# Optimization experiments

Measured on AMD Instinct MI355X. Metric: run time of the kernel, lower is better.

The kernel has to match this reference:

```python
import jax, jax.numpy as jnp
import numpy as np

N_EMBD = 768
N_HEAD = 12
HEAD_DIM = N_EMBD // N_HEAD


def setup_inputs() -> dict:
    key = jax.random.key(0)
    ks = jax.random.split(key, 5)
    B, T, C = 1, 4096, N_EMBD
    s = 1.0 / np.sqrt(C)
    return {
        "x": jax.random.normal(ks[0], (B, T, C), dtype=jnp.float32),
        "wq": jax.random.normal(ks[1], (C, C), dtype=jnp.float32) * s,
        "wk": jax.random.normal(ks[2], (C, C), dtype=jnp.float32) * s,
        "wv": jax.random.normal(ks[3], (C, C), dtype=jnp.float32) * s,
        "wo": jax.random.normal(ks[4], (C, C), dtype=jnp.float32) * s,
    }


def reference(x, wq, wk, wv, wo):
    B, T, C = x.shape
    H, D = N_HEAD, HEAD_DIM
    # projections: torch Linear(y = x @ W^T); weights stored as (out, in)
    q = (x @ wq.T).reshape(B, T, H, D).transpose(0, 2, 1, 3)  # B H T D
    k = (x @ wk.T).reshape(B, T, H, D).transpose(0, 2, 1, 3)
    v = (x @ wv.T).reshape(B, T, H, D).transpose(0, 2, 1, 3)
    scale = 1.0 / jnp.sqrt(jnp.asarray(D, dtype=x.dtype))
    attn = jnp.einsum("bhtd,bhsd->bhts", q, k) * scale  # B H T T
    causal = jnp.tril(jnp.ones((T, T), dtype=bool))
    attn = jnp.where(causal, attn, -jnp.inf)
    attn = jax.nn.softmax(attn, axis=-1)
    out = jnp.einsum("bhts,bhsd->bhtd", attn, v)  # B H T D
    out = out.transpose(0, 2, 1, 3).reshape(B, T, C)
    return out @ wo.T
```

## Files before the change

kernel.cpp:

```cpp
#include <hip/hip_runtime.h>


#define T_SEQ 4096
#define C_EMB 768
#define NH    12
#define HD    64

typedef __attribute__((ext_vector_type(8))) short bf16x8;
typedef __attribute__((ext_vector_type(4))) float floatx4;

#define QSCALE 0.18033688011112042f

__device__ __forceinline__ unsigned short f2bf(float f) {
  union { float f; unsigned u; } v; v.f = f;
  unsigned r = v.u + 0x7fffu + ((v.u >> 16) & 1u);
  return (unsigned short)(r >> 16);
}
__device__ __forceinline__ unsigned short f2bf_rhu(float f) {
  union { float f; unsigned u; } v; v.f = f;
  return (unsigned short)((v.u + 0x8000u) >> 16);
}
__device__ __forceinline__ float bf2f(unsigned short h) {
  union { unsigned u; float f; } v; v.u = ((unsigned)h) << 16;
  return v.f;
}

__device__ __forceinline__ void gload_lds16(const void* gptr, void* ldsptr) {
  __builtin_amdgcn_global_load_lds(
      (const __attribute__((address_space(1))) unsigned int*)gptr,
      (__attribute__((address_space(3))) unsigned int*)ldsptr,
      16, 0, 0);
}

__global__ void cast_all_kernel(const float* __restrict__ x,
                                const float* __restrict__ wq,
                                const float* __restrict__ wk,
                                const float* __restrict__ wv,
                                const float* __restrict__ wo,
                                unsigned short* __restrict__ dst) {
  const int GX = (T_SEQ * C_EMB) / 4;
  const int GW = (C_EMB * C_EMB) / 4;
  int i = blockIdx.x * blockDim.x + threadIdx.x;
  const float* src; int local;
  if (i < GX) { src = x; local = i; }
  else {
    int t = i - GX; int w = t / GW; local = t - w * GW;
    src = (w == 0) ? wq : (w == 1) ? wk : (w == 2) ? wv : wo;
  }
  float4 f = reinterpret_cast<const float4*>(src)[local];
  ushort4 u;
  u.x = f2bf(f.x); u.y = f2bf(f.y); u.z = f2bf(f.z); u.w = f2bf(f.w);
  reinterpret_cast<ushort4*>(dst)[i] = u;
}

__global__ __launch_bounds__(256) void gemm_qkv(
    const unsigned short* __restrict__ A,
    const unsigned short* __restrict__ B,
    unsigned short* __restrict__ Qb,
    unsigned short* __restrict__ Kb,
    unsigned short* __restrict__ Vt) {
  constexpr int K = 768, BM = 128, BK = 32;
  __shared__ __align__(16) unsigned short As[BM * BK];
  __shared__ __align__(16) unsigned short Bs[BM * BK];
  const int tid = threadIdx.x;
  const int wave = tid >> 6, lane = tid & 63;
  const int lm = lane & 15, lq = lane >> 4;
  const int sw2 = (lm ^ (lm >> 2)) & 3;
  const int m0 = blockIdx.x * BM, n0 = blockIdx.y * BM;
  const int wm = (wave & 1) * 64, wn = (wave >> 1) * 64;
  floatx4 acc[4][4] = {};

  for (int k0 = 0; k0 < K; k0 += BK) {
#pragma unroll
    for (int i = 0; i < 2; i++) {
      int idx = (wave * 2 + i) * 64 + lane;
      int row = idx >> 2;
      int ch = (idx & 3) ^ ((row ^ (row >> 2)) & 3);
      gload_lds16(A + (size_t)(m0 + row) * K + k0 + ch * 8, (char*)As + idx * 16);
      gload_lds16(B + (size_t)(n0 + row) * K + k0 + ch * 8, (char*)Bs + idx * 16);
    }
    __syncthreads();
    bf16x8 af[4], bfr[4];
#pragma unroll
    for (int i = 0; i < 4; i++)
      af[i] = *(const bf16x8*)(As + (wm + i * 16 + lm) * BK + ((lq ^ sw2) * 8));
#pragma unroll
    for (int j = 0; j < 4; j++)
      bfr[j] = *(const bf16x8*)(Bs + (wn + j * 16 + lm) * BK + ((lq ^ sw2) * 8));
#pragma unroll
    for (int i = 0; i < 4; i++)
#pragma unroll
      for (int j = 0; j < 4; j++)
        acc[i][j] = __builtin_amdgcn_mfma_f32_16x16x32_bf16(af[i], bfr[j], acc[i][j], 0, 0, 0);
    __syncthreads();
  }

  const int which = n0 / C_EMB;
  if (which < 2) {
    unsigned short* tgt = (which == 0) ? Qb : Kb;
    const float sc = (which == 0) ? QSCALE : 1.0f;
#pragma unroll
    for (int i = 0; i < 4; i++)
#pragma unroll
      for (int j = 0; j < 4; j++) {
        int n = n0 - which * C_EMB + wn + j * 16 + lm;
        int h = n >> 6, d = n & 63;
#pragma unroll
        for (int r = 0; r < 4; r++) {
          int m = m0 + wm + i * 16 + lq * 4 + r;
          tgt[(((size_t)h * T_SEQ + m) << 6) + d] = f2bf(acc[i][j][r] * sc);
        }
      }
  } else {
#pragma unroll
    for (int i = 0; i < 4; i++)
#pragma unroll
      for (int j = 0; j < 4; j++) {
        int n = n0 - 2 * C_EMB + wn + j * 16 + lm;
        int h = n >> 6, d = n & 63;
        int m = m0 + wm + i * 16 + lq * 4;
        ushort4 pk;
        pk.x = f2bf(acc[i][j][0]); pk.y = f2bf(acc[i][j][1]);
        pk.z = f2bf(acc[i][j][2]); pk.w = f2bf(acc[i][j][3]);
        *(ushort4*)(Vt + ((size_t)(h * HD + d)) * T_SEQ + m) = pk;
      }
  }
}

__global__ __launch_bounds__(256, 4) void attn_kernel(
    const unsigned short* __restrict__ Q,
    const unsigned short* __restrict__ K,
    const unsigned short* __restrict__ Vt,
    unsigned short* __restrict__ Op0,
    unsigned short* __restrict__ Op1,
    float* __restrict__ lpart) {
  constexpr int BS = 64, PS = 72;
  __shared__ __align__(16) unsigned short Ks[BS * HD];
  __shared__ __align__(16) unsigned short Vs[HD * BS];
  __shared__ __align__(16) unsigned short Ps[4 * 32 * PS];
  const int bid = blockIdx.x;
  const int h = bid % NH;
  const int z = bid / NH;
  const int qt = (T_SEQ / 128 - 1) - (z >> 1);
  const int c = z & 1;
  const int q0 = qt * 128;
  const int sb = c ? (qt + 1) : 0;
  const int se = c ? (2 * qt + 2) : (qt + 1);

  const int tid = threadIdx.x;
  const int wave = tid >> 6, lane = tid & 63;
  const int lm = lane & 15, lq = lane >> 4;
  const unsigned short* Qh = Q + (size_t)h * T_SEQ * HD;
  const unsigned short* Kh = K + (size_t)h * T_SEQ * HD;
  const unsigned short* Vh = Vt + (size_t)h * HD * T_SEQ;
  const int qrow_base = q0 + wave * 32;
  unsigned short* Pw = Ps + wave * 32 * PS;
  const int swz = lm & 7;

  bf16x8 qf[2][2];
#pragma unroll
  for (int m = 0; m < 2; m++)
#pragma unroll
    for (int kk = 0; kk < 2; kk++)
      qf[m][kk] = *(const bf16x8*)(Qh + (size_t)(qrow_base + m * 16 + lm) * HD + kk * 32 + lq * 8);

  float rsum[2][4] = {};
  floatx4 o_acc[2][4] = {};

  auto stage = [&](int s0) {
#pragma unroll
    for (int i = 0; i < 2; i++) {
      int idx = (wave * 2 + i) * 64 + lane;
      int row = idx >> 3;
      int ch = (idx & 7) ^ (row & 7);
      gload_lds16(Kh + (size_t)(s0 + row) * HD + ch * 8, (char*)Ks + idx * 16);
      gload_lds16(Vh + (size_t)row * T_SEQ + s0 + ch * 8, (char*)Vs + idx * 16);
    }
  };

  stage(sb * BS);
  for (int it = sb; it < se; ++it) {
    const int s0 = it * BS;
    __syncthreads();

    floatx4 sa[2][4] = {};
#pragma unroll
    for (int kk = 0; kk < 2; kk++)
#pragma unroll
      for (int j = 0; j < 4; j++) {
        int row = j * 16 + lm;
        bf16x8 kf = *(const bf16x8*)(Ks + (row * 8 + ((kk * 4 + lq) ^ swz)) * 8);
#pragma unroll
        for (int m = 0; m < 2; m++)
          sa[m][j] = __builtin_amdgcn_mfma_f32_16x16x32_bf16(qf[m][kk], kf, sa[m][j], 0, 0, 0);
      }

    if (s0 >= q0) {
#pragma unroll
      for (int m = 0; m < 2; m++)
#pragma unroll
        for (int j = 0; j < 4; j++) {
          int scol = s0 + j * 16 + lm;
#pragma unroll
          for (int r = 0; r < 4; r++) {
            int qrow = qrow_base + m * 16 + lq * 4 + r;
            if (scol > qrow) sa[m][j][r] = -1e30f;
          }
        }
    }

#pragma unroll
    for (int m = 0; m < 2; m++)
#pragma unroll
      for (int j = 0; j < 4; j++)
#pragma unroll
        for (int r = 0; r < 4; r++) {
          float p = __builtin_amdgcn_exp2f(sa[m][j][r]);
          rsum[m][r] += p;
          Pw[(m * 16 + lq * 4 + r) * PS + j * 16 + lm] = f2bf_rhu(p);
        }

#pragma unroll
    for (int kk = 0; kk < 2; kk++) {
      bf16x8 pf[2];
#pragma unroll
      for (int m = 0; m < 2; m++)
        pf[m] = *(const bf16x8*)(Pw + (m * 16 + lm) * PS + kk * 32 + lq * 8);
#pragma unroll
      for (int jd = 0; jd < 4; jd++) {
        int row = jd * 16 + lm;
        bf16x8 vf = *(const bf16x8*)(Vs + (row * 8 + ((kk * 4 + lq) ^ swz)) * 8);
#pragma unroll
        for (int m = 0; m < 2; m++)
          o_acc[m][jd] = __builtin_amdgcn_mfma_f32_16x16x32_bf16(pf[m], vf, o_acc[m][jd], 0, 0, 0);
      }
    }

    if (it + 1 < se) {
      __syncthreads();
      stage(s0 + BS);
    }
  }

  unsigned short* Oc = c ? Op1 : Op0;
  float* lc = lpart + (size_t)c * NH * T_SEQ;
#pragma unroll
  for (int m = 0; m < 2; m++)
#pragma unroll
    for (int r = 0; r < 4; r++) {
      float s = rsum[m][r];
      s += __shfl_xor(s, 1);
      s += __shfl_xor(s, 2);
      s += __shfl_xor(s, 4);
      s += __shfl_xor(s, 8);
      int t = qrow_base + m * 16 + lq * 4 + r;
      if (lm == 0) lc[h * T_SEQ + t] = s;
#pragma unroll
      for (int jd = 0; jd < 4; jd++)
        Oc[((size_t)h * T_SEQ + t) * HD + jd * 16 + lm] = f2bf(o_acc[m][jd][r]);
    }
}

__global__ void combine_kernel(const unsigned short* __restrict__ Op0,
                               const unsigned short* __restrict__ Op1,
                               const float* __restrict__ lpart,
                               unsigned short* __restrict__ Ob) {
  int idx = blockIdx.x * blockDim.x + threadIdx.x;
  int d4 = idx & 15;
  int t = (idx >> 4) & (T_SEQ - 1);
  int h = idx >> 16;
  float l = lpart[h * T_SEQ + t] + lpart[NH * T_SEQ + h * T_SEQ + t];
  float inv = 1.0f / l;
  ushort4 a = reinterpret_cast<const ushort4*>(Op0)[idx];
  ushort4 b = reinterpret_cast<const ushort4*>(Op1)[idx];
  ushort4 u;
  u.x = f2bf((bf2f(a.x) + bf2f(b.x)) * inv);
  u.y = f2bf((bf2f(a.y) + bf2f(b.y)) * inv);
  u.z = f2bf((bf2f(a.z) + bf2f(b.z)) * inv);
  u.w = f2bf((bf2f(a.w) + bf2f(b.w)) * inv);
  *(ushort4*)(Ob + (size_t)t * C_EMB + h * HD + d4 * 4) = u;
}

__global__ __launch_bounds__(256) void gemm_out(
    const unsigned short* __restrict__ A,
    const unsigned short* __restrict__ B,
    float* __restrict__ Out) {
  constexpr int K = 768, BM = 128, BK = 32;
  __shared__ __align__(16) unsigned short As[BM * BK];
  __shared__ __align__(16) unsigned short Bs[BM * BK];
  const int tid = threadIdx.x;
  const int wave = tid >> 6, lane = tid & 63;
  const int lm = lane & 15, lq = lane >> 4;
  const int sw2 = (lm ^ (lm >> 2)) & 3;
  const int m0 = blockIdx.x * BM, n0 = blockIdx.y * BM;
  const int wm = (wave & 1) * 64, wn = (wave >> 1) * 64;
  floatx4 acc[4][4] = {};

  for (int k0 = 0; k0 < K; k0 += BK) {
#pragma unroll
    for (int i = 0; i < 2; i++) {
      int idx = (wave * 2 + i) * 64 + lane;
      int row = idx >> 2;
      int ch = (idx & 3) ^ ((row ^ (row >> 2)) & 3);
      gload_lds16(A + (size_t)(m0 + row) * K + k0 + ch * 8, (char*)As + idx * 16);
      gload_lds16(B + (size_t)(n0 + row) * K + k0 + ch * 8, (char*)Bs + idx * 16);
    }
    __syncthreads();
    bf16x8 af[4], bfr[4];
#pragma unroll
    for (int i = 0; i < 4; i++)
      af[i] = *(const bf16x8*)(As + (wm + i * 16 + lm) * BK + ((lq ^ sw2) * 8));
#pragma unroll
    for (int j = 0; j < 4; j++)
      bfr[j] = *(const bf16x8*)(Bs + (wn + j * 16 + lm) * BK + ((lq ^ sw2) * 8));
#pragma unroll
    for (int i = 0; i < 4; i++)
#pragma unroll
      for (int j = 0; j < 4; j++)
        acc[i][j] = __builtin_amdgcn_mfma_f32_16x16x32_bf16(af[i], bfr[j], acc[i][j], 0, 0, 0);
    __syncthreads();
  }
#pragma unroll
  for (int i = 0; i < 4; i++)
#pragma unroll
    for (int j = 0; j < 4; j++)
#pragma unroll
      for (int r = 0; r < 4; r++) {
        int m = m0 + wm + i * 16 + lq * 4 + r;
        int n = n0 + wn + j * 16 + lm;
        Out[(size_t)m * C_EMB + n] = acc[i][j][r];
      }
}

extern "C" void kernel_launch(void* const* d_in, const int* in_sizes, int n_in,
                              void* d_out, int out_size, void* d_ws, size_t ws_size,
                              hipStream_t stream) {
  const float* x  = (const float*)d_in[0];
  const float* wq = (const float*)d_in[1];
  const float* wk = (const float*)d_in[2];
  const float* wv = (const float*)d_in[3];
  const float* wo = (const float*)d_in[4];
  float* out = (float*)d_out;

  const size_t XN = (size_t)T_SEQ * C_EMB;
  const size_t WN = (size_t)C_EMB * C_EMB;
  unsigned short* base = (unsigned short*)d_ws;

  unsigned short* Xb   = base;
  unsigned short* Wqkv = base + XN;
  unsigned short* Wob  = base + XN + 3 * WN;
  unsigned short* Qb   = base + XN + 4 * WN;
  unsigned short* Kb   = Qb + XN;
  unsigned short* Vt   = Kb + XN;
  unsigned short* Op1  = Vt + XN;
  unsigned short* Op0  = base;
  float* lpart = (float*)(base + XN);
  unsigned short* Ob   = Qb;

  const int ngroups = (int)((XN + 4 * WN) / 4);
  cast_all_kernel<<<dim3(ngroups / 256), 256, 0, stream>>>(x, wq, wk, wv, wo, Xb);

  gemm_qkv<<<dim3(T_SEQ / 128, 2304 / 128), 256, 0, stream>>>(Xb, Wqkv, Qb, Kb, Vt);

  attn_kernel<<<dim3((T_SEQ / 128) * 2 * NH), 256, 0, stream>>>(Qb, Kb, Vt, Op0, Op1, lpart);
  combine_kernel<<<dim3((int)(XN / 4) / 256), 256, 0, stream>>>(Op0, Op1, lpart, Ob);
  gemm_out<<<dim3(T_SEQ / 128, C_EMB / 128), 256, 0, stream>>>(Ob, Wob, out);
}
```

Baseline: 189.2 us.

## Split causal attention KV range into four chunks with fp32 partials

The attention kernel now splits each query tile's key range into four chunks instead of two, launching twice as many blocks. Each chunk writes fp32 partial outputs and row sums, and a new combine kernel adds the non-empty chunks and normalises. The aim is better load balance and occupancy across CUs for the causal workload. In exchange the partials move more memory traffic (fp32, four copies) and need a larger workspace, with a fallback to the old two-way path when the workspace is too small.

```diff
diff --git a/kernel.cpp b/kernel.cpp
--- a/kernel.cpp
+++ b/kernel.cpp
@@ -127,7 +127,133 @@
   }
 }
 
-__global__ __launch_bounds__(256, 4) void attn_kernel(
+struct AttnState {
+  float rsum[2][4];
+  floatx4 o_acc[2][4];
+};
+
+template <typename EpilogueFn>
+__device__ __forceinline__ void attn_body(
+    const unsigned short* __restrict__ Q,
+    const unsigned short* __restrict__ K,
+    const unsigned short* __restrict__ Vt,
+    int h, int q0, int sb, int se,
+    unsigned short* Ks, unsigned short* Vs, unsigned short* Ps,
+    EpilogueFn epi) {
+  constexpr int BS = 64, PS = 72;
+  const int tid = threadIdx.x;
+  const int wave = tid >> 6, lane = tid & 63;
+  const int lm = lane & 15, lq = lane >> 4;
+  const unsigned short* Qh = Q + (size_t)h * T_SEQ * HD;
+  const unsigned short* Kh = K + (size_t)h * T_SEQ * HD;
+  const unsigned short* Vh = Vt + (size_t)h * HD * T_SEQ;
+  const int qrow_base = q0 + wave * 32;
+  unsigned short* Pw = Ps + wave * 32 * PS;
+  const int swz = lm & 7;
+
+  bf16x8 qf[2][2];
+#pragma unroll
+  for (int m = 0; m < 2; m++)
+#pragma unroll
+    for (int kk = 0; kk < 2; kk++)
+      qf[m][kk] = *(const bf16x8*)(Qh + (size_t)(qrow_base + m * 16 + lm) * HD + kk * 32 + lq * 8);
+
+  AttnState st;
+#pragma unroll
+  for (int m = 0; m < 2; m++)
+#pragma unroll
+    for (int r = 0; r < 4; r++) { st.rsum[m][r] = 0.f; st.o_acc[m][r] = floatx4{0.f,0.f,0.f,0.f}; }
+
+  auto stage = [&](int s0) {
+#pragma unroll
+    for (int i = 0; i < 2; i++) {
+      int idx = (wave * 2 + i) * 64 + lane;
+      int row = idx >> 3;
+      int ch = (idx & 7) ^ (row & 7);
+      gload_lds16(Kh + (size_t)(s0 + row) * HD + ch * 8, (char*)Ks + idx * 16);
+      gload_lds16(Vh + (size_t)row * T_SEQ + s0 + ch * 8, (char*)Vs + idx * 16);
+    }
+  };
+
+  stage(sb * BS);
+  for (int it = sb; it < se; ++it) {
+    const int s0 = it * BS;
+    __syncthreads();
+
+    floatx4 sa[2][4] = {};
+#pragma unroll
+    for (int kk = 0; kk < 2; kk++)
+#pragma unroll
+      for (int j = 0; j < 4; j++) {
+        int row = j * 16 + lm;
+        bf16x8 kf = *(const bf16x8*)(Ks + (row * 8 + ((kk * 4 + lq) ^ swz)) * 8);
+#pragma unroll
+        for (int m = 0; m < 2; m++)
+          sa[m][j] = __builtin_amdgcn_mfma_f32_16x16x32_bf16(qf[m][kk], kf, sa[m][j], 0, 0, 0);
+      }
+
+    if (s0 >= q0) {
+#pragma unroll
+      for (int m = 0; m < 2; m++)
+#pragma unroll
+        for (int j = 0; j < 4; j++) {
+          int scol = s0 + j * 16 + lm;
+#pragma unroll
+          for (int r = 0; r < 4; r++) {
+            int qrow = qrow_base + m * 16 + lq * 4 + r;
+            if (scol > qrow) sa[m][j][r] = -1e30f;
+          }
+        }
+    }
+
+#pragma unroll
+    for (int m = 0; m < 2; m++)
+#pragma unroll
+      for (int j = 0; j < 4; j++)
+#pragma unroll
+        for (int r = 0; r < 4; r++) {
+          float p = __builtin_amdgcn_exp2f(sa[m][j][r]);
+          st.rsum[m][r] += p;
+          Pw[(m * 16 + lq * 4 + r) * PS + j * 16 + lm] = f2bf_rhu(p);
+        }
+
+#pragma unroll
+    for (int kk = 0; kk < 2; kk++) {
+      bf16x8 pf[2];
+#pragma unroll
+      for (int m = 0; m < 2; m++)
+        pf[m] = *(const bf16x8*)(Pw + (m * 16 + lm) * PS + kk * 32 + lq * 8);
+#pragma unroll
+      for (int jd = 0; jd < 4; jd++) {
+        int row = jd * 16 + lm;
+        bf16x8 vf = *(const bf16x8*)(Vs + (row * 8 + ((kk * 4 + lq) ^ swz)) * 8);
+#pragma unroll
+        for (int m = 0; m < 2; m++)
+          st.o_acc[m][jd] = __builtin_amdgcn_mfma_f32_16x16x32_bf16(pf[m], vf, st.o_acc[m][jd], 0, 0, 0);
+      }
+    }
+
+    if (it + 1 < se) {
+      __syncthreads();
+      stage(s0 + BS);
+    }
+  }
+
+#pragma unroll
+  for (int m = 0; m < 2; m++)
+#pragma unroll
+    for (int r = 0; r < 4; r++) {
+      float s = st.rsum[m][r];
+      s += __shfl_xor(s, 1);
+      s += __shfl_xor(s, 2);
+      s += __shfl_xor(s, 4);
+      s += __shfl_xor(s, 8);
+      st.rsum[m][r] = s;
+    }
+  epi(st, qrow_base, lm, lq);
+}
+
+__global__ __launch_bounds__(256, 4) void attn_kernel2(
     const unsigned short* __restrict__ Q,
     const unsigned short* __restrict__ K,
     const unsigned short* __restrict__ Vt,
@@ -147,124 +273,27 @@
   const int sb = c ? (qt + 1) : 0;
   const int se = c ? (2 * qt + 2) : (qt + 1);
 
-  const int tid = threadIdx.x;
-  const int wave = tid >> 6, lane = tid & 63;
-  const int lm = lane & 15, lq = lane >> 4;
-  const unsigned short* Qh = Q + (size_t)h * T_SEQ * HD;
-  const unsigned short* Kh = K + (size_t)h * T_SEQ * HD;
-  const unsigned short* Vh = Vt + (size_t)h * HD * T_SEQ;
-  const int qrow_base = q0 + wave * 32;
-  unsigned short* Pw = Ps + wave * 32 * PS;
-  const int swz = lm & 7;
-
-  bf16x8 qf[2][2];
-#pragma unroll
-  for (int m = 0; m < 2; m++)
-#pragma unroll
-    for (int kk = 0; kk < 2; kk++)
-      qf[m][kk] = *(const bf16x8*)(Qh + (size_t)(qrow_base + m * 16 + lm) * HD + kk * 32 + lq * 8);
-
-  float rsum[2][4] = {};
-  floatx4 o_acc[2][4] = {};
-
-  auto stage = [&](int s0) {
-#pragma unroll
-    for (int i = 0; i < 2; i++) {
-      int idx = (wave * 2 + i) * 64 + lane;
-      int row = idx >> 3;
-      int ch = (idx & 7) ^ (row & 7);
-      gload_lds16(Kh + (size_t)(s0 + row) * HD + ch * 8, (char*)Ks + idx * 16);
-      gload_lds16(Vh + (size_t)row * T_SEQ + s0 + ch * 8, (char*)Vs + idx * 16);
-    }
-  };
-
-  stage(sb * BS);
-  for (int it = sb; it < se; ++it) {
-    const int s0 = it * BS;
-    __syncthreads();
-
-    floatx4 sa[2][4] = {};
-#pragma unroll
-    for (int kk = 0; kk < 2; kk++)
-#pragma unroll
-      for (int j = 0; j < 4; j++) {
-        int row = j * 16 + lm;
-        bf16x8 kf = *(const bf16x8*)(Ks + (row * 8 + ((kk * 4 + lq) ^ swz)) * 8);
-#pragma unroll
-        for (int m = 0; m < 2; m++)
-          sa[m][j] = __builtin_amdgcn_mfma_f32_16x16x32_bf16(qf[m][kk], kf, sa[m][j], 0, 0, 0);
-      }
-
-    if (s0 >= q0) {
-#pragma unroll
-      for (int m = 0; m < 2; m++)
-#pragma unroll
-        for (int j = 0; j < 4; j++) {
-          int scol = s0 + j * 16 + lm;
-#pragma unroll
-          for (int r = 0; r < 4; r++) {
-            int qrow = qrow_base + m * 16 + lq * 4 + r;
-            if (scol > qrow) sa[m][j][r] = -1e30f;
-          }
-        }
-    }
-
-#pragma unroll
-    for (int m = 0; m < 2; m++)
-#pragma unroll
-      for (int j = 0; j < 4; j++)
-#pragma unroll
-        for (int r = 0; r < 4; r++) {
-          float p = __builtin_amdgcn_exp2f(sa[m][j][r]);
-          rsum[m][r] += p;
-          Pw[(m * 16 + lq * 4 + r) * PS + j * 16 + lm] = f2bf_rhu(p);
-        }
-
-#pragma unroll
-    for (int kk = 0; kk < 2; kk++) {
-      bf16x8 pf[2];
-#pragma unroll
-      for (int m = 0; m < 2; m++)
-        pf[m] = *(const bf16x8*)(Pw + (m * 16 + lm) * PS + kk * 32 + lq * 8);
-#pragma unroll
-      for (int jd = 0; jd < 4; jd++) {
-        int row = jd * 16 + lm;
-        bf16x8 vf = *(const bf16x8*)(Vs + (row * 8 + ((kk * 4 + lq) ^ swz)) * 8);
-#pragma unroll
-        for (int m = 0; m < 2; m++)
-          o_acc[m][jd] = __builtin_amdgcn_mfma_f32_16x16x32_bf16(pf[m], vf, o_acc[m][jd], 0, 0, 0);
-      }
-    }
-
-    if (it + 1 < se) {
-      __syncthreads();
-      stage(s0 + BS);
-    }
-  }
-
   unsigned short* Oc = c ? Op1 : Op0;
   float* lc = lpart + (size_t)c * NH * T_SEQ;
-#pragma unroll
-  for (int m = 0; m < 2; m++)
-#pragma unroll
-    for (int r = 0; r < 4; r++) {
-      float s = rsum[m][r];
-      s += __shfl_xor(s, 1);
-      s += __shfl_xor(s, 2);
-      s += __shfl_xor(s, 4);
-      s += __shfl_xor(s, 8);
-      int t = qrow_base + m * 16 + lq * 4 + r;
-      if (lm == 0) lc[h * T_SEQ + t] = s;
-#pragma unroll
-      for (int jd = 0; jd < 4; jd++)
-        Oc[((size_t)h * T_SEQ + t) * HD + jd * 16 + lm] = f2bf(o_acc[m][jd][r]);
-    }
-}
-
-__global__ void combine_kernel(const unsigned short* __restrict__ Op0,
-                               const unsigned short* __restrict__ Op1,
-                               const float* __restrict__ lpart,
-                               unsigned short* __restrict__ Ob) {
+  attn_body(Q, K, Vt, h, q0, sb, se, Ks, Vs, Ps,
+    [&](const AttnState& st, int qrow_base, int lm, int lq) {
+#pragma unroll
+      for (int m = 0; m < 2; m++)
+#pragma unroll
+        for (int r = 0; r < 4; r++) {
+          int t = qrow_base + m * 16 + lq * 4 + r;
+          if (lm == 0) lc[h * T_SEQ + t] = st.rsum[m][r];
+#pragma unroll
+          for (int jd = 0; jd < 4; jd++)
+            Oc[((size_t)h * T_SEQ + t) * HD + jd * 16 + lm] = f2bf(st.o_acc[m][jd][r]);
+        }
+    });
+}
+
+__global__ void combine_kernel2(const unsigned short* __restrict__ Op0,
+                                const unsigned short* __restrict__ Op1,
+                                const float* __restrict__ lpart,
+                                unsigned short* __restrict__ Ob) {
   int idx = blockIdx.x * blockDim.x + threadIdx.x;
   int d4 = idx & 15;
   int t = (idx >> 4) & (T_SEQ - 1);
@@ -281,6 +310,71 @@
   *(ushort4*)(Ob + (size_t)t * C_EMB + h * HD + d4 * 4) = u;
 }
 
+__global__ __launch_bounds__(256, 4) void attn_kernel4(
+    const unsigned short* __restrict__ Q,
+    const unsigned short* __restrict__ K,
+    const unsigned short* __restrict__ Vt,
+    float* __restrict__ Opart,
+    float* __restrict__ lpart) {
+  constexpr int BS = 64, PS = 72;
+  __shared__ __align__(16) unsigned short Ks[BS * HD];
+  __shared__ __align__(16) unsigned short Vs[HD * BS];
+  __shared__ __align__(16) unsigned short Ps[4 * 32 * PS];
+  const int bid = blockIdx.x;
+  const int h = bid % NH;
+  const int z = bid / NH;
+  const int qt = (T_SEQ / 128 - 1) - (z >> 2);
+  const int c = z & 3;
+  const int q0 = qt * 128;
+  const int n = 2 * qt + 2;
+  const int sb = (n * c) >> 2, se = (n * (c + 1)) >> 2;
+  if (sb == se) return;
+
+  const size_t CN = (size_t)NH * T_SEQ * HD;
+  float* Oc = Opart + (size_t)c * CN;
+  float* lc = lpart + (size_t)c * NH * T_SEQ;
+  attn_body(Q, K, Vt, h, q0, sb, se, Ks, Vs, Ps,
+    [&](const AttnState& st, int qrow_base, int lm, int lq) {
+#pragma unroll
+      for (int m = 0; m < 2; m++)
+#pragma unroll
+        for (int r = 0; r < 4; r++) {
+          int t = qrow_base + m * 16 + lq * 4 + r;
+          if (lm == 0) lc[h * T_SEQ + t] = st.rsum[m][r];
+#pragma unroll
+          for (int jd = 0; jd < 4; jd++)
+            Oc[((size_t)h * T_SEQ + t) * HD + jd * 16 + lm] = st.o_acc[m][jd][r];
+        }
+    });
+}
+
+__global__ void combine_kernel4(const float* __restrict__ Opart,
+                                const float* __restrict__ lpart,
+                                unsigned short* __restrict__ Ob) {
+  int idx = blockIdx.x * blockDim.x + threadIdx.x;
+  int d4 = idx & 15;
+  int t = (idx >> 4) & (T_SEQ - 1);
+  int h = idx >> 16;
+  const int qt = t >> 7;
+  const int n = 2 * qt + 2;
+  const size_t CN4 = (size_t)NH * T_SEQ * HD / 4;
+  float4 o = make_float4(0.f, 0.f, 0.f, 0.f);
+  float l = 0.f;
+#pragma unroll
+  for (int c = 0; c < 4; c++) {
+    if (((n * c) >> 2) != ((n * (c + 1)) >> 2)) {
+      float4 p = reinterpret_cast<const float4*>(Opart)[c * CN4 + idx];
+      o.x += p.x; o.y += p.y; o.z += p.z; o.w += p.w;
+      l += lpart[c * NH * T_SEQ + h * T_SEQ + t];
+    }
+  }
+  float inv = 1.0f / l;
+  ushort4 u;
+  u.x = f2bf(o.x * inv); u.y = f2bf(o.y * inv);
+  u.z = f2bf(o.z * inv); u.w = f2bf(o.w * inv);
+  *(ushort4*)(Ob + (size_t)t * C_EMB + h * HD + d4 * 4) = u;
+}
+
 __global__ __launch_bounds__(256) void gemm_out(
     const unsigned short* __restrict__ A,
     const unsigned short* __restrict__ B,
@@ -352,17 +446,28 @@
   unsigned short* Qb   = base + XN + 4 * WN;
   unsigned short* Kb   = Qb + XN;
   unsigned short* Vt   = Kb + XN;
-  unsigned short* Op1  = Vt + XN;
-  unsigned short* Op0  = base;
-  float* lpart = (float*)(base + XN);
+  unsigned short* tail = Vt + XN;
   unsigned short* Ob   = Qb;
+
+  const size_t needA = 29884416ull + 4ull * XN * 4ull + 4ull * NH * T_SEQ * 4ull;
 
   const int ngroups = (int)((XN + 4 * WN) / 4);
   cast_all_kernel<<<dim3(ngroups / 256), 256, 0, stream>>>(x, wq, wk, wv, wo, Xb);
 
   gemm_qkv<<<dim3(T_SEQ / 128, 2304 / 128), 256, 0, stream>>>(Xb, Wqkv, Qb, Kb, Vt);
 
-  attn_kernel<<<dim3((T_SEQ / 128) * 2 * NH), 256, 0, stream>>>(Qb, Kb, Vt, Op0, Op1, lpart);
-  combine_kernel<<<dim3((int)(XN / 4) / 256), 256, 0, stream>>>(Op0, Op1, lpart, Ob);
+  if (ws_size >= needA) {
+    float* Opart4 = (float*)tail;
+    float* lpart4 = Opart4 + 4 * XN;
+    attn_kernel4<<<dim3((T_SEQ / 128) * 4 * NH), 256, 0, stream>>>(Qb, Kb, Vt, Opart4, lpart4);
+    combine_kernel4<<<dim3((int)(XN / 4) / 256), 256, 0, stream>>>(Opart4, lpart4, Ob);
+  } else {
+    unsigned short* Op0 = base;
+    unsigned short* Op1 = tail;
+    float* lpart = (float*)(base + XN);
+    attn_kernel2<<<dim3((T_SEQ / 128) * 2 * NH), 256, 0, stream>>>(Qb, Kb, Vt, Op0, Op1, lpart);
+    combine_kernel2<<<dim3((int)(XN / 4) / 256), 256, 0, stream>>>(Op0, Op1, lpart, Ob);
+  }
+
   gemm_out<<<dim3(T_SEQ / 128, C_EMB / 128), 256, 0, stream>>>(Ob, Wob, out);
 }
```

Measured after the change: 185.5 us. 2.0% less time.
